# Performance work log

Measured on AMD Instinct MI355X. Metric: run time of the kernel, lower is better.

## Reference

```python
import jax, jax.numpy as jnp
import numpy as np

B, N, IN, HID, OUT = 64, 256, 7, 64, 32
DEG = 32
NT = B * N          # total nodes per side
E = NT * DEG        # intra-graph edges per side
TAU = 1.0
MAX_ITER = 10
EPS = 1e-5          # InstanceNorm2d eps


def setup_inputs() -> dict:
    key = jax.random.key(0)
    ks = jax.random.split(key, 12)

    def edges(k):
        # random intra-graph edges: local indices in [0, N) plus per-graph offset
        loc = jax.random.randint(k, (2, B, N * DEG), 0, N)
        off = (jnp.arange(B) * N)[None, :, None]
        return (loc + off).reshape(2, -1).astype(jnp.int64)

    def lin(k, fi, fo):
        return jax.random.normal(k, (fi, fo), jnp.float32) / np.float32(np.sqrt(fi))

    return {
        "x1": jax.random.normal(ks[0], (NT, IN), jnp.float32),
        "x2": jax.random.normal(ks[1], (NT, IN), jnp.float32),
        "edge1": edges(ks[2]),
        "edge2": edges(ks[3]),
        "Wl1": lin(ks[4], IN, HID), "Wr1": lin(ks[5], IN, HID),
        "bl1": jnp.zeros((HID,), jnp.float32), "br1": jnp.zeros((HID,), jnp.float32),
        "att1": jax.random.normal(ks[6], (HID,), jnp.float32) * 0.1,
        "bias1": jnp.zeros((HID,), jnp.float32),
        "Wl2": lin(ks[7], HID, OUT), "Wr2": lin(ks[8], HID, OUT),
        "bl2": jnp.zeros((OUT,), jnp.float32), "br2": jnp.zeros((OUT,), jnp.float32),
        "att2": jax.random.normal(ks[9], (OUT,), jnp.float32) * 0.1,
        "bias2": jnp.zeros((OUT,), jnp.float32),
        "gamma": jnp.ones((1,), jnp.float32),
        "beta": jnp.zeros((1,), jnp.float32),
    }


def _gatv2(x, src, dst, Wl, bl, Wr, br, att, bias):
    # PyG GATv2Conv, heads=1: score = att . leaky_relu(lin_l(x_j) + lin_r(x_i))
    xl = x @ Wl + bl  # source transform
    xr = x @ Wr + br  # target transform
    e = jax.nn.leaky_relu(xl[src] + xr[dst], 0.2)     # [E, D]
    score = e @ att                                    # [E]
    smax = jax.ops.segment_max(score, dst, num_segments=NT)
    ex = jnp.exp(score - smax[dst])
    den = jax.ops.segment_sum(ex, dst, num_segments=NT)
    alpha = ex / den[dst]
    out = jax.ops.segment_sum(alpha[:, None] * xl[src], dst, num_segments=NT)
    return out + bias


def _encode(x, edge, params):
    # add self loops (PyG add_self_loops=True default)
    loops = jnp.arange(NT)
    src = jnp.concatenate([edge[0], loops])
    dst = jnp.concatenate([edge[1], loops])
    h = jax.nn.relu(_gatv2(x, src, dst, *params[0]))
    return _gatv2(h, src, dst, *params[1])


def _soft_topk(sim_n):
    # AFAT-style differentiable top-k: OT between flattened scores and
    # {min, max} anchors with marginals [(n-k)/n, k/n], k = N2 per pair.
    n = N * N
    k = N
    flat = sim_n.reshape(B, n)
    mn = flat.min(axis=1, keepdims=True)
    mx = flat.max(axis=1, keepdims=True)
    dist = jnp.stack([flat - mn, mx - flat], axis=-1)  # [B, n, 2] (|s-min|,|s-max|)
    logK = -dist / TAU
    log_row = -jnp.log(jnp.float32(n))
    log_col = jnp.log(jnp.array([(n - k) / n, k / n], jnp.float32))
    for i in range(MAX_ITER):
        if i % 2 == 0:  # row normalization to uniform 1/n
            logK = logK - jax.scipy.special.logsumexp(logK, axis=-1, keepdims=True) + log_row
        else:           # column normalization to [(n-k)/n, k/n]
            logK = logK - jax.scipy.special.logsumexp(logK, axis=1, keepdims=True) + log_col[None, None, :]
    soft = jnp.clip(jnp.exp(logK[:, :, 1]) * n, 0.0, 1.0)  # selection probability per entry
    return soft.reshape(B, N, N)


def reference(x1, x2, edge1, edge2, Wl1, Wr1, bl1, br1, att1, bias1,
              Wl2, Wr2, bl2, br2, att2, bias2, gamma, beta):
    params = ((Wl1, bl1, Wr1, br1, att1, bias1), (Wl2, bl2, Wr2, br2, att2, bias2))
    h1 = _encode(x1, edge1, params).reshape(B, N, OUT)
    h2 = _encode(x2, edge2, params).reshape(B, N, OUT)
    sim = jnp.einsum('bnd,bmd->bnm', h1, h2)
    # InstanceNorm2d(1, affine=True): normalize each pair's sim matrix
    mu = sim.mean(axis=(1, 2), keepdims=True)
    var = sim.var(axis=(1, 2), keepdims=True)
    sim_n = gamma[0] * (sim - mu) * jax.lax.rsqrt(var + EPS) + beta[0]
    return _soft_topk(sim_n)  # soft_S stacked over the batch, [B, N, N]
```

## Files before the change

kernel.cpp:

```cpp
#include <hip/hip_runtime.h>

#define NB 64
#define NN 256
#define IND 7
#define HIDD 64
#define OUTD 32
#define EPG 8192
#define ETOT 524288
#define CAPQ 2600
#define SRCPAD 2624

typedef _Float16 f16;
typedef f16 f16x2 __attribute__((ext_vector_type(2)));
typedef f16 f16x4 __attribute__((ext_vector_type(4)));
typedef f16 f16x8 __attribute__((ext_vector_type(8)));
typedef float f32x4 __attribute__((ext_vector_type(4)));

__device__ __forceinline__ float bsum16(float v, float* rb){
#pragma unroll
  for (int o = 32; o > 0; o >>= 1) v += __shfl_xor(v, o, 64);
  __syncthreads();
  if ((threadIdx.x & 63) == 0) rb[threadIdx.x >> 6] = v;
  __syncthreads();
  float s = 0.f;
#pragma unroll
  for (int i = 0; i < 16; i++) s += rb[i];
  return s;
}
__device__ __forceinline__ float bmin16(float v, float* rb){
#pragma unroll
  for (int o = 32; o > 0; o >>= 1) v = fminf(v, __shfl_xor(v, o, 64));
  __syncthreads();
  if ((threadIdx.x & 63) == 0) rb[threadIdx.x >> 6] = v;
  __syncthreads();
  float s = rb[0];
#pragma unroll
  for (int i = 1; i < 16; i++) s = fminf(s, rb[i]);
  return s;
}
__device__ __forceinline__ float bmax16(float v, float* rb){
#pragma unroll
  for (int o = 32; o > 0; o >>= 1) v = fmaxf(v, __shfl_xor(v, o, 64));
  __syncthreads();
  if ((threadIdx.x & 63) == 0) rb[threadIdx.x >> 6] = v;
  __syncthreads();
  float s = rb[0];
#pragma unroll
  for (int i = 1; i < 16; i++) s = fmaxf(s, rb[i]);
  return s;
}

__device__ __forceinline__ f16x2 lrelu2(f16x2 s){
  const f16x2 k = {(f16)0.2f, (f16)0.2f};
  return __builtin_elementwise_max(s, s * k);
}
__device__ __forceinline__ f16x2 shfl_h2(f16x2 v, int lane){
  int i = __builtin_bit_cast(int, v);
  i = __shfl(i, lane, 64);
  return __builtin_bit_cast(f16x2, i);
}

__global__ __launch_bounds__(512, 4) void gat1(
    const float* __restrict__ x1, const float* __restrict__ x2,
    const int* __restrict__ e1, const int* __restrict__ e2,
    const float* __restrict__ Wl, const float* __restrict__ Wr,
    const float* __restrict__ bl, const float* __restrict__ br,
    const float* __restrict__ att, const float* __restrict__ bias,
    f16* __restrict__ hmid,
    int* __restrict__ meta, unsigned char* __restrict__ srcs)
{
  __shared__ __align__(16) f16 xl_s[256 * 72];
  __shared__ float sc_s[CAPQ];
  __shared__ unsigned int src_su[SRCPAD / 4];
  __shared__ int deg_s[64], start_s[64], cnt_s[64];
  __shared__ unsigned char perm[64];
  unsigned char* src_s = (unsigned char*)src_su;

  const int bid = blockIdx.x;
  const int gs = bid & 127, lo = (bid >> 7) * 64;
  const int side = gs >> 6, g = gs & 63;
  const float* x = side ? x2 : x1;
  const int* eb = side ? e2 : e1;
  const int* es = eb + g * EPG;
  const int* ed = eb + ETOT + g * EPG;
  const int t = threadIdx.x;

  if (t < 64) deg_s[t] = 0;

  unsigned short epk[17];
  int nE = 0;
#pragma unroll
  for (int i = 0; i < 17; i++){
    int e = t + i * 512;
    if (e < EPG + 256){
      int sl, dl;
      if (e < EPG){ sl = es[e] & 255; dl = ed[e] & 255; }
      else { sl = dl = e - EPG; }
      epk[i] = (unsigned short)((dl << 8) | sl);
      nE = i + 1;
    }
  }

  {
    const int node = t >> 1, dh = t & 1;
    float xv[IND];
    const float* xr_ = x + (g * 256 + node) * IND;
#pragma unroll
    for (int k = 0; k < IND; k++) xv[k] = xr_[k];
#pragma unroll
    for (int ch = 0; ch < 4; ch++){
      f16x8 o;
#pragma unroll
      for (int j = 0; j < 8; j++){
        int dd = dh * 32 + ch * 8 + j;
        float a = bl[dd];
#pragma unroll
        for (int k = 0; k < IND; k++) a = fmaf(xv[k], Wl[k * HIDD + dd], a);
        o[j] = (f16)a;
      }
      *(f16x8*)&xl_s[node * 72 + dh * 32 + ch * 8] = o;
    }
  }
  __syncthreads();

#pragma unroll
  for (int i = 0; i < 17; i++) if (i < nE){
    int r = (epk[i] >> 8) - lo;
    if ((unsigned)r < 64u) atomicAdd(&deg_s[r], 1);
  }
  __syncthreads();
  if (t < 64){
    int v = deg_s[t], s = v;
#pragma unroll
    for (int off = 1; off < 64; off <<= 1){
      int u = __shfl_up(s, off, 64);
      if (t >= off) s += u;
    }
    start_s[t] = s - v;
    cnt_s[t] = s - v;
    meta[bid * 128 + t] = s - v;
    meta[bid * 128 + 64 + t] = v;
    int r = 0;
#pragma unroll 8
    for (int j = 0; j < 64; j++){
      int dj = deg_s[j];
      r += (dj < v) || (dj == v && j < t);
    }
    perm[r] = (unsigned char)t;
  }
  __syncthreads();
#pragma unroll
  for (int i = 0; i < 17; i++) if (i < nE){
    int dl = epk[i] >> 8, r = dl - lo;
    if ((unsigned)r < 64u){
      int p = atomicAdd(&cnt_s[r], 1);
      if (p < CAPQ) src_s[p] = (unsigned char)(epk[i] & 255);
    }
  }
  __syncthreads();
  {
    int ttl = start_s[63] + deg_s[63];
    if (ttl > CAPQ) ttl = CAPQ;
    unsigned int* gsrc = (unsigned int*)(srcs + (size_t)bid * SRCPAD);
    int nw = (ttl + 3) >> 2;
    for (int i = t; i < nw; i += 512) gsrc[i] = src_su[i];
  }

  const int pairi = perm[t >> 3], sub = t & 7, ln = lo + pairi;
  f16x2 m[4], am[4];
  {
    float xv[IND];
    const float* xq = x + (g * 256 + ln) * IND;
#pragma unroll
    for (int k = 0; k < IND; k++) xv[k] = xq[k];
#pragma unroll
    for (int c = 0; c < 4; c++){
#pragma unroll
      for (int u = 0; u < 2; u++){
        int dd = sub * 8 + 2 * c + u;
        float a = br[dd];
#pragma unroll
        for (int k = 0; k < IND; k++) a = fmaf(xv[k], Wr[k * HIDD + dd], a);
        m[c][u] = (f16)a;
        am[c][u] = (f16)att[dd];
      }
    }
  }
  f16x2 xrh[32], atth[32];
  {
    const int base = (t & 63) & ~7;
#pragma unroll
    for (int ss = 0; ss < 8; ss++){
#pragma unroll
      for (int c = 0; c < 4; c++){
        xrh[ss * 4 + c] = shfl_h2(m[c], base + ss);
        atth[ss * 4 + c] = shfl_h2(am[c], base + ss);
      }
    }
  }

  const int s0 = start_s[pairi];
  int sE = s0 + deg_s[pairi];
  if (sE > CAPQ) sE = CAPQ;
  float ssum = 0.f;
  for (int idx = s0 + sub; idx < sE; idx += 8){
    int sl = src_s[idx];
    const f16x8* rp = (const f16x8*)&xl_s[(unsigned)sl * 72];
    float accs[4] = {0.f, 0.f, 0.f, 0.f};
#pragma unroll
    for (int blk = 0; blk < 8; blk++){
      f16x8 rv = rp[blk];
#pragma unroll
      for (int u = 0; u < 4; u++){
        f16x2 v = {rv[2 * u], rv[2 * u + 1]};
        v = v + xrh[blk * 4 + u];
        accs[u] = __builtin_amdgcn_fdot2(lrelu2(v), atth[blk * 4 + u], accs[u], false);
      }
    }
    float w = __expf((accs[0] + accs[1]) + (accs[2] + accs[3]));
    sc_s[idx] = w;
    ssum += w;
  }
  ssum += __shfl_xor(ssum, 1, 64);
  ssum += __shfl_xor(ssum, 2, 64);
  ssum += __shfl_xor(ssum, 4, 64);
  float inv = 1.f / ssum;
  float acc[8];
#pragma unroll
  for (int c = 0; c < 8; c++) acc[c] = 0.f;
  {
    int sl = (s0 < sE) ? src_s[s0] : 0;
    f16x8 row = *(const f16x8*)&xl_s[(unsigned)sl * 72 + sub * 8];
    for (int idx = s0; idx < sE; idx++){
      int sln = (idx + 1 < sE) ? src_s[idx + 1] : 0;
      f16x8 rown = *(const f16x8*)&xl_s[(unsigned)sln * 72 + sub * 8];
      float w = sc_s[idx];
#pragma unroll
      for (int c = 0; c < 8; c++) acc[c] = fmaf(w, (float)row[c], acc[c]);
      row = rown;
    }
  }
  f16x8 o;
#pragma unroll
  for (int c = 0; c < 8; c++)
    o[c] = (f16)fmaxf(acc[c] * inv + bias[sub * 8 + c], 0.f);
  *(f16x8*)(hmid + (size_t)(gs * 256 + ln) * 64 + sub * 8) = o;
}

__global__ __launch_bounds__(512, 4) void gat2(
    const int* __restrict__ meta, const unsigned char* __restrict__ srcs,
    const f16* __restrict__ hmid,
    const float* __restrict__ Wl, const float* __restrict__ Wr,
    const float* __restrict__ bl, const float* __restrict__ br,
    const float* __restrict__ att, const float* __restrict__ bias,
    f16* __restrict__ hout)
{
  __shared__ __align__(16) f16 xl_s[256 * 40];
  __shared__ __align__(16) f16 xr_s[64 * 40];
  __shared__ float sc_s[CAPQ];
  __shared__ unsigned int src_su[SRCPAD / 4];
  __shared__ int start_s[64], deg_s[64];
  __shared__ unsigned char perm[64];
  unsigned char* src_s = (unsigned char*)src_su;

  const int bid = blockIdx.x;
  const int gs = bid & 127, lo = (bid >> 7) * 64;
  const int t = threadIdx.x;

  if (t < 64){
    start_s[t] = meta[bid * 128 + t];
    deg_s[t] = meta[bid * 128 + 64 + t];
  }
  {
    int ttl = meta[bid * 128 + 63] + meta[bid * 128 + 64 + 63];
    if (ttl > CAPQ) ttl = CAPQ;
    const unsigned int* gsrc = (const unsigned int*)(srcs + (size_t)bid * SRCPAD);
    int nw = (ttl + 3) >> 2;
    for (int i = t; i < nw; i += 512) src_su[i] = gsrc[i];
  }

  {
    const int w = t >> 6, lane = t & 63;
    const int m = lane & 15, quad = lane >> 4;
    f16x8 a[2][2];
#pragma unroll
    for (int ti = 0; ti < 2; ti++){
      const f16* arow = hmid + (size_t)(gs * 256 + (2 * w + ti) * 16 + m) * 64;
      a[ti][0] = *(const f16x8*)(arow + quad * 8);
      a[ti][1] = *(const f16x8*)(arow + 32 + quad * 8);
    }
#pragma unroll
    for (int H = 0; H < 2; H++){
      const int n = H * 16 + m;
      f16x8 b0, b1;
#pragma unroll
      for (int j = 0; j < 8; j++){
        b0[j] = (f16)Wl[(quad * 8 + j) * 32 + n];
        b1[j] = (f16)Wl[(32 + quad * 8 + j) * 32 + n];
      }
      const float bv = bl[n];
#pragma unroll
      for (int ti = 0; ti < 2; ti++){
        f32x4 acc = {0.f, 0.f, 0.f, 0.f};
        acc = __builtin_amdgcn_mfma_f32_16x16x32_f16(a[ti][0], b0, acc, 0, 0, 0);
        acc = __builtin_amdgcn_mfma_f32_16x16x32_f16(a[ti][1], b1, acc, 0, 0, 0);
#pragma unroll
        for (int r = 0; r < 4; r++)
          xl_s[((2 * w + ti) * 16 + quad * 4 + r) * 40 + n] = (f16)(acc[r] + bv);
      }
    }
    if (w < 4){
      const f16* arow = hmid + (size_t)(gs * 256 + lo + w * 16 + m) * 64;
      f16x8 c0 = *(const f16x8*)(arow + quad * 8);
      f16x8 c1 = *(const f16x8*)(arow + 32 + quad * 8);
#pragma unroll
      for (int H = 0; H < 2; H++){
        const int n = H * 16 + m;
        f16x8 b0, b1;
#pragma unroll
        for (int j = 0; j < 8; j++){
          b0[j] = (f16)Wr[(quad * 8 + j) * 32 + n];
          b1[j] = (f16)Wr[(32 + quad * 8 + j) * 32 + n];
        }
        const float bv = br[n];
        f32x4 acc = {0.f, 0.f, 0.f, 0.f};
        acc = __builtin_amdgcn_mfma_f32_16x16x32_f16(c0, b0, acc, 0, 0, 0);
        acc = __builtin_amdgcn_mfma_f32_16x16x32_f16(c1, b1, acc, 0, 0, 0);
#pragma unroll
        for (int r = 0; r < 4; r++)
          xr_s[(w * 16 + quad * 4 + r) * 40 + n] = (f16)(acc[r] + bv);
      }
    }
  }
  __syncthreads();
  if (t < 64){
    int v = deg_s[t], r = 0;
#pragma unroll 8
    for (int j = 0; j < 64; j++){
      int dj = deg_s[j];
      r += (dj < v) || (dj == v && j < t);
    }
    perm[r] = (unsigned char)t;
  }
  __syncthreads();

  const int pairi = perm[t >> 3], sub = t & 7, ln = lo + pairi;
  f16x2 xrh[16], atth[16];
  {
    const f16x8* xrp = (const f16x8*)&xr_s[pairi * 40];
#pragma unroll
    for (int q = 0; q < 4; q++){
      f16x8 v = xrp[q];
#pragma unroll
      for (int u = 0; u < 4; u++){
        xrh[q * 4 + u][0] = v[2 * u];
        xrh[q * 4 + u][1] = v[2 * u + 1];
      }
    }
#pragma unroll
    for (int i = 0; i < 16; i++){
      atth[i][0] = (f16)att[2 * i];
      atth[i][1] = (f16)att[2 * i + 1];
    }
  }

  const int s0 = start_s[pairi];
  int sE = s0 + deg_s[pairi];
  if (sE > CAPQ) sE = CAPQ;
  float ssum = 0.f;
  for (int idx = s0 + sub; idx < sE; idx += 8){
    int sl = src_s[idx];
    const f16x8* rp = (const f16x8*)&xl_s[(unsigned)sl * 40];
    float accs[4] = {0.f, 0.f, 0.f, 0.f};
#pragma unroll
    for (int blk = 0; blk < 4; blk++){
      f16x8 rv = rp[blk];
#pragma unroll
      for (int u = 0; u < 4; u++){
        f16x2 v = {rv[2 * u], rv[2 * u + 1]};
        v = v + xrh[blk * 4 + u];
        accs[u] = __builtin_amdgcn_fdot2(lrelu2(v), atth[blk * 4 + u], accs[u], false);
      }
    }
    float w = __expf((accs[0] + accs[1]) + (accs[2] + accs[3]));
    sc_s[idx] = w;
    ssum += w;
  }
  ssum += __shfl_xor(ssum, 1, 64);
  ssum += __shfl_xor(ssum, 2, 64);
  ssum += __shfl_xor(ssum, 4, 64);
  float inv = 1.f / ssum;

  float acc[4];
#pragma unroll
  for (int c = 0; c < 4; c++) acc[c] = 0.f;
  {
    int sl = (s0 < sE) ? src_s[s0] : 0;
    f16x4 row = *(const f16x4*)&xl_s[(unsigned)sl * 40 + sub * 4];
    for (int idx = s0; idx < sE; idx++){
      int sln = (idx + 1 < sE) ? src_s[idx + 1] : 0;
      f16x4 rown = *(const f16x4*)&xl_s[(unsigned)sln * 40 + sub * 4];
      float w = sc_s[idx];
#pragma unroll
      for (int c = 0; c < 4; c++) acc[c] = fmaf(w, (float)row[c], acc[c]);
      row = rown;
    }
  }
  f16x4 o;
#pragma unroll
  for (int c = 0; c < 4; c++)
    o[c] = (f16)(acc[c] * inv + bias[sub * 4 + c]);
  *(f16x4*)(hout + (size_t)(gs * 256 + ln) * 32 + sub * 4) = o;
}

__global__ __launch_bounds__(1024) void sinkk(
    const f16* __restrict__ H,
    const float* __restrict__ gamma, const float* __restrict__ beta,
    float* __restrict__ res)
{
  __shared__ float rb[16];
  __shared__ unsigned int hist[8192];
  const int b = blockIdx.x, t = threadIdx.x;
  const int w = t >> 6, lane = t & 63;
  const int m = lane & 15, quad = lane >> 4;

  const f16* h1 = H + (size_t)b * 256 * 32;
  const f16* h2 = H + (size_t)(64 + b) * 256 * 32;

  f16x8 av = *(const f16x8*)(h1 + (size_t)(w * 16 + m) * 32 + quad * 8);
  f32x4 c[16];
#pragma unroll
  for (int j = 0; j < 16; j++){
    f16x8 bv = *(const f16x8*)(h2 + (size_t)(j * 16 + m) * 32 + quad * 8);
    f32x4 z = {0.f, 0.f, 0.f, 0.f};
    c[j] = __builtin_amdgcn_mfma_f32_16x16x32_f16(av, bv, z, 0, 0, 0);
  }

  float sm = 0.f, s2 = 0.f, mn = 3.0e38f, mx = -3.0e38f;
#pragma unroll
  for (int j = 0; j < 16; j++)
#pragma unroll
    for (int r = 0; r < 4; r++){
      float s = c[j][r];
      sm += s; s2 = fmaf(s, s, s2);
      mn = fminf(mn, s); mx = fmaxf(mx, s);
    }
  sm = bsum16(sm, rb);
  s2 = bsum16(s2, rb);
  mn = bmin16(mn, rb);
  mx = bmax16(mx, rb);

  const float mu = sm * (1.f / 65536.f);
  const float var = s2 * (1.f / 65536.f) - mu * mu;
  const float a = gamma[0] * rsqrtf(var + 1e-5f);
  const float cc = beta[0] - a * mu;
  float mnn = a * mn + cc, mxn = a * mx + cc;
  if (a < 0.f){ float tmp = mnn; mnn = mxn; mxn = tmp; }
  const float al = 2.f * a;
  const float be = 2.f * cc - mnn - mxn;
  const float R = fmaxf(mxn - mnn, 1e-12f);
  const float binscale = 4096.f / R;

  for (int i = t; i < 8192; i += 1024) hist[i] = 0u;
  __syncthreads();
#pragma unroll
  for (int j = 0; j < 16; j++)
#pragma unroll
    for (int r = 0; r < 4; r++){
      float z = fmaf(al, c[j][r], be);
      int bi = (int)fmaf(z, binscale, 4096.f);
      bi = min(max(bi, 0), 8191);
      atomicAdd(&hist[bi], 1u);
    }
  __syncthreads();

  const float wbin = R * (1.f / 4096.f);
  float ebs[8], cnts[8];
#pragma unroll
  for (int j = 0; j < 8; j++){
    float zc = fmaf((float)(t * 8 + j) + 0.5f, wbin, -R);
    ebs[j] = __expf(-zc);
    cnts[j] = (float)hist[t * 8 + j];
  }

  float D = 0.f, S = 256.f, eD = 1.f;
  for (int p = 0; p < 5; p++){
    float loc = 0.f;
#pragma unroll
    for (int j = 0; j < 8; j++)
      loc += cnts[j] / (1.f + ebs[j] * eD);
    S = bsum16(loc, rb);
    if (p < 4){
      D += -5.5412635f  + __logf(65536.f - S) - __logf(S);
      eD = __expf(-D);
    }
  }
  if (t == 0){
    res[b * 4 + 0] = al;
    res[b * 4 + 1] = be + D;
    res[b * 4 + 2] = 256.f / S;
  }
}

__global__ __launch_bounds__(1024) void outk(
    const f16* __restrict__ H, const float* __restrict__ res,
    float* __restrict__ out)
{
  const int b = blockIdx.x & 63, q = blockIdx.x >> 6, t = threadIdx.x;
  const int w = t >> 6, lane = t & 63;
  const int m = lane & 15, quad = lane >> 4;
  const int rowT = q * 64 + (w & 3) * 16;
  const int colB = (w >> 2) * 64;

  const float al = res[b * 4 + 0];
  const float beD = res[b * 4 + 1];
  const float scale = res[b * 4 + 2];

  const f16* h1 = H + (size_t)b * 256 * 32;
  const f16* h2 = H + (size_t)(64 + b) * 256 * 32;

  f16x8 av = *(const f16x8*)(h1 + (size_t)(rowT + m) * 32 + quad * 8);
  float* ob = out + (size_t)b * 65536;
#pragma unroll
  for (int jj = 0; jj < 4; jj++){
    f16x8 bv = *(const f16x8*)(h2 + (size_t)(colB + jj * 16 + m) * 32 + quad * 8);
    f32x4 z = {0.f, 0.f, 0.f, 0.f};
    f32x4 c = __builtin_amdgcn_mfma_f32_16x16x32_f16(av, bv, z, 0, 0, 0);
#pragma unroll
    for (int r = 0; r < 4; r++){
      float zz = fmaf(al, c[r], beD);
      float v = fminf(scale / (1.f + __expf(-zz)), 1.f);
      ob[(rowT + quad * 4 + r) * 256 + colB + jj * 16 + m] = v;
    }
  }
}

extern "C" void kernel_launch(void* const* d_in, const int* in_sizes, int n_in,
                              void* d_out, int out_size, void* d_ws, size_t ws_size,
                              hipStream_t stream)
{
  const float* x1   = (const float*)d_in[0];
  const float* x2   = (const float*)d_in[1];
  const int*   e1   = (const int*)d_in[2];
  const int*   e2   = (const int*)d_in[3];
  const float* Wl1  = (const float*)d_in[4];
  const float* Wr1  = (const float*)d_in[5];
  const float* bl1  = (const float*)d_in[6];
  const float* br1  = (const float*)d_in[7];
  const float* att1 = (const float*)d_in[8];
  const float* bias1= (const float*)d_in[9];
  const float* Wl2  = (const float*)d_in[10];
  const float* Wr2  = (const float*)d_in[11];
  const float* bl2  = (const float*)d_in[12];
  const float* br2  = (const float*)d_in[13];
  const float* att2 = (const float*)d_in[14];
  const float* bias2= (const float*)d_in[15];
  const float* gamma= (const float*)d_in[16];
  const float* beta = (const float*)d_in[17];

  char* ws = (char*)d_ws;
  f16* hfin = (f16*)ws;
  f16* hmid = (f16*)(ws + (size_t)2 * 1024 * 1024);
  int* meta = (int*)(ws + (size_t)6 * 1024 * 1024);
  unsigned char* srcs = (unsigned char*)(ws + (size_t)6 * 1024 * 1024 + 512 * 128 * 4);
  float* res = (float*)(ws + (size_t)8 * 1024 * 1024);
  float* out = (float*)d_out;

  gat1<<<512, 512, 0, stream>>>(x1, x2, e1, e2, Wl1, Wr1, bl1, br1, att1, bias1,
                                hmid, meta, srcs);
  gat2<<<512, 512, 0, stream>>>(meta, srcs, hmid, Wl2, Wr2, bl2, br2, att2, bias2, hfin);
  sinkk<<<64, 1024, 0, stream>>>(hfin, gamma, beta, res);
  outk<<<256, 1024, 0, stream>>>(hfin, res, out);
}
```

Before: 176.3 us.

## Fuse sinkhorn stats and output kernels with redundant per-quarter recompute

Merges the per-batch statistics/histogram Sinkhorn kernel and the output kernel into one kernel launched with 256 blocks. Each of the four blocks per batch recomputes the full similarity matrix, histogram and normalization constant, then writes only its quarter of the rows. The four separate block reductions are also folded into one combined shuffle pass with a single barrier, and the histogram clear is overlapped with it. This removes a launch and the round trip through global memory, at the cost of doing the sinkhorn work four times over.

Measured after the change: 172.9 us. Within noise of the previous version (-1.9%).

```diff
diff --git a/kernel.cpp b/kernel.cpp
--- a/kernel.cpp
+++ b/kernel.cpp
@@ -25,28 +25,6 @@
   float s = 0.f;
 #pragma unroll
   for (int i = 0; i < 16; i++) s += rb[i];
-  return s;
-}
-__device__ __forceinline__ float bmin16(float v, float* rb){
-#pragma unroll
-  for (int o = 32; o > 0; o >>= 1) v = fminf(v, __shfl_xor(v, o, 64));
-  __syncthreads();
-  if ((threadIdx.x & 63) == 0) rb[threadIdx.x >> 6] = v;
-  __syncthreads();
-  float s = rb[0];
-#pragma unroll
-  for (int i = 1; i < 16; i++) s = fminf(s, rb[i]);
-  return s;
-}
-__device__ __forceinline__ float bmax16(float v, float* rb){
-#pragma unroll
-  for (int o = 32; o > 0; o >>= 1) v = fmaxf(v, __shfl_xor(v, o, 64));
-  __syncthreads();
-  if ((threadIdx.x & 63) == 0) rb[threadIdx.x >> 6] = v;
-  __syncthreads();
-  float s = rb[0];
-#pragma unroll
-  for (int i = 1; i < 16; i++) s = fmaxf(s, rb[i]);
   return s;
 }
 
@@ -413,14 +391,15 @@
   *(f16x4*)(hout + (size_t)(gs * 256 + ln) * 32 + sub * 4) = o;
 }
 
-__global__ __launch_bounds__(1024) void sinkk(
+__global__ __launch_bounds__(1024) void sinkout(
     const f16* __restrict__ H,
     const float* __restrict__ gamma, const float* __restrict__ beta,
-    float* __restrict__ res)
+    float* __restrict__ out)
 {
   __shared__ float rb[16];
+  __shared__ __align__(16) float rb4s[64];
   __shared__ unsigned int hist[8192];
-  const int b = blockIdx.x, t = threadIdx.x;
+  const int b = blockIdx.x & 63, q = blockIdx.x >> 6, t = threadIdx.x;
   const int w = t >> 6, lane = t & 63;
   const int m = lane & 15, quad = lane >> 4;
 
@@ -445,10 +424,27 @@
       sm += s; s2 = fmaf(s, s, s2);
       mn = fminf(mn, s); mx = fmaxf(mx, s);
     }
-  sm = bsum16(sm, rb);
-  s2 = bsum16(s2, rb);
-  mn = bmin16(mn, rb);
-  mx = bmax16(mx, rb);
+#pragma unroll
+  for (int o = 32; o > 0; o >>= 1){
+    sm += __shfl_xor(sm, o, 64);
+    s2 += __shfl_xor(s2, o, 64);
+    mn = fminf(mn, __shfl_xor(mn, o, 64));
+    mx = fmaxf(mx, __shfl_xor(mx, o, 64));
+  }
+  if (lane == 0){
+    rb4s[w * 4 + 0] = sm; rb4s[w * 4 + 1] = s2;
+    rb4s[w * 4 + 2] = mn; rb4s[w * 4 + 3] = mx;
+  }
+  for (int i = t; i < 8192; i += 1024) hist[i] = 0u;
+  __syncthreads();
+  sm = 0.f; s2 = 0.f; mn = 3.0e38f; mx = -3.0e38f;
+#pragma unroll
+  for (int i = 0; i < 16; i++){
+    sm += rb4s[i * 4 + 0];
+    s2 += rb4s[i * 4 + 1];
+    mn = fminf(mn, rb4s[i * 4 + 2]);
+    mx = fmaxf(mx, rb4s[i * 4 + 3]);
+  }
 
   const float mu = sm * (1.f / 65536.f);
   const float var = s2 * (1.f / 65536.f) - mu * mu;
@@ -461,8 +457,6 @@
   const float R = fmaxf(mxn - mnn, 1e-12f);
   const float binscale = 4096.f / R;
 
-  for (int i = t; i < 8192; i += 1024) hist[i] = 0u;
-  __syncthreads();
 #pragma unroll
   for (int j = 0; j < 16; j++)
 #pragma unroll
@@ -495,42 +489,19 @@
       eD = __expf(-D);
     }
   }
-  if (t == 0){
-    res[b * 4 + 0] = al;
-    res[b * 4 + 1] = be + D;
-    res[b * 4 + 2] = 256.f / S;
-  }
-}
-
-__global__ __launch_bounds__(1024) void outk(
-    const f16* __restrict__ H, const float* __restrict__ res,
-    float* __restrict__ out)
-{
-  const int b = blockIdx.x & 63, q = blockIdx.x >> 6, t = threadIdx.x;
-  const int w = t >> 6, lane = t & 63;
-  const int m = lane & 15, quad = lane >> 4;
-  const int rowT = q * 64 + (w & 3) * 16;
-  const int colB = (w >> 2) * 64;
-
-  const float al = res[b * 4 + 0];
-  const float beD = res[b * 4 + 1];
-  const float scale = res[b * 4 + 2];
-
-  const f16* h1 = H + (size_t)b * 256 * 32;
-  const f16* h2 = H + (size_t)(64 + b) * 256 * 32;
-
-  f16x8 av = *(const f16x8*)(h1 + (size_t)(rowT + m) * 32 + quad * 8);
-  float* ob = out + (size_t)b * 65536;
-#pragma unroll
-  for (int jj = 0; jj < 4; jj++){
-    f16x8 bv = *(const f16x8*)(h2 + (size_t)(colB + jj * 16 + m) * 32 + quad * 8);
-    f32x4 z = {0.f, 0.f, 0.f, 0.f};
-    f32x4 c = __builtin_amdgcn_mfma_f32_16x16x32_f16(av, bv, z, 0, 0, 0);
-#pragma unroll
-    for (int r = 0; r < 4; r++){
-      float zz = fmaf(al, c[r], beD);
-      float v = fminf(scale / (1.f + __expf(-zz)), 1.f);
-      ob[(rowT + quad * 4 + r) * 256 + colB + jj * 16 + m] = v;
+
+  const float beD = be + D;
+  const float scale = 256.f / S;
+  if ((w >> 2) == q){
+    float* ob = out + (size_t)b * 65536;
+#pragma unroll
+    for (int j = 0; j < 16; j++){
+#pragma unroll
+      for (int r = 0; r < 4; r++){
+        float zz = fmaf(al, c[j][r], beD);
+        float v = fminf(scale / (1.f + __expf(-zz)), 1.f);
+        ob[(w * 16 + quad * 4 + r) * 256 + j * 16 + m] = v;
+      }
     }
   }
 }
@@ -563,12 +534,10 @@
   f16* hmid = (f16*)(ws + (size_t)2 * 1024 * 1024);
   int* meta = (int*)(ws + (size_t)6 * 1024 * 1024);
   unsigned char* srcs = (unsigned char*)(ws + (size_t)6 * 1024 * 1024 + 512 * 128 * 4);
-  float* res = (float*)(ws + (size_t)8 * 1024 * 1024);
   float* out = (float*)d_out;
 
   gat1<<<512, 512, 0, stream>>>(x1, x2, e1, e2, Wl1, Wr1, bl1, br1, att1, bias1,
                                 hmid, meta, srcs);
   gat2<<<512, 512, 0, stream>>>(meta, srcs, hmid, Wl2, Wr2, bl2, br2, att2, bias2, hfin);
-  sinkk<<<64, 1024, 0, stream>>>(hfin, gamma, beta, res);
-  outk<<<256, 1024, 0, stream>>>(hfin, res, out);
-}
+  sinkout<<<256, 1024, 0, stream>>>(hfin, gamma, beta, out);
+}
```
